# Kernel tuning notes

Hardware: AMD Instinct MI355X
Metric: run time of the kernel (lower is better)

Reference implementation:

```python
import jax, jax.numpy as jnp
import numpy as np

BANK_FILTERS = 64
DIM = 128
KSIZE = 3
BATCH = 256


def setup_inputs() -> dict:
    key = jax.random.key(0)
    k1, k2 = jax.random.split(key)
    bank_request = jax.random.normal(k1, (BATCH, BANK_FILTERS), dtype=jnp.float32)
    weight = jax.random.normal(k2, (BANK_FILTERS, DIM, DIM, KSIZE, KSIZE), dtype=jnp.float32)
    return {"bank_request": bank_request, "weight": weight}


def reference(bank_request, weight):
    # softmax over filter bank, then weighted sum of filters -> per-sample kernel
    probs = jax.nn.softmax(bank_request, axis=1)          # (B, F)
    Fb, D1, D2, K1, K2 = weight.shape
    # express as a single GEMM over the filter axis instead of broadcast-mul-reduce
    w2d = weight.reshape(Fb, D1 * D2 * K1 * K2)           # (F, D*D*k*k)
    kernel = probs @ w2d                                   # (B, D*D*k*k)
    return kernel.reshape(bank_request.shape[0], D1, D2, K1, K2)
```

## Files before the change

### kernel.cpp

```cpp
#include <hip/hip_runtime.h>
#include <math.h>

#define BATCH 256
#define FB    64
#define NCOL  147456
#define TPB   256
#define BT    32

#define FMA4(a, s, w) do { \
    (a).x = fmaf((s), (w).x, (a).x); \
    (a).y = fmaf((s), (w).y, (a).y); \
    (a).z = fmaf((s), (w).z, (a).z); \
    (a).w = fmaf((s), (w).w, (a).w); \
} while (0)

__global__ void softmax_rows(const float* __restrict__ x, float* __restrict__ p) {
    const int b = blockIdx.x;
    const int lane = threadIdx.x;
    float v = x[b * FB + lane];
    float m = v;
#pragma unroll
    for (int o = 32; o > 0; o >>= 1) m = fmaxf(m, __shfl_xor(m, o));
    float e = __expf(v - m);
    float s = e;
#pragma unroll
    for (int o = 32; o > 0; o >>= 1) s += __shfl_xor(s, o);
    p[b * FB + lane] = e / s;
}

__global__ __launch_bounds__(TPB, 2) void bank_gemm(
        const float* __restrict__ W, const float* __restrict__ P,
        float* __restrict__ out) {
    __shared__ float pt[FB * BT];

    const int tid = threadIdx.x;
    const int bg  = blockIdx.y;

    for (int i = tid; i < FB * BT; i += TPB) {
        const int f = i & (FB - 1);
        const int b = i >> 6;
        pt[f * BT + b] = P[bg * (FB * BT) + i];
    }
    __syncthreads();

    const int ncol4 = NCOL / 4;
    const float4* Wv = (const float4*)W;
    const int c4 = blockIdx.x * TPB + tid;

    float4 acc[BT];
#pragma unroll
    for (int b = 0; b < BT; ++b) acc[b] = make_float4(0.f, 0.f, 0.f, 0.f);

    float4 w = Wv[c4];
    for (int f = 0; f < FB; ++f) {
        float4 wn = w;
        if (f + 1 < FB) wn = Wv[(f + 1) * ncol4 + c4];
        const float4* p4 = (const float4*)&pt[f * BT];
#pragma unroll
        for (int q = 0; q < BT / 4; ++q) {
            const float4 p = p4[q];
            FMA4(acc[4 * q + 0], p.x, w);
            FMA4(acc[4 * q + 1], p.y, w);
            FMA4(acc[4 * q + 2], p.z, w);
            FMA4(acc[4 * q + 3], p.w, w);
        }
        w = wn;
    }

    float4* Ov = (float4*)out;
    const long long obase = (long long)(bg * BT) * ncol4 + c4;
#pragma unroll
    for (int b = 0; b < BT; ++b) {
        Ov[obase + (long long)b * ncol4] = acc[b];
    }
}

extern "C" void kernel_launch(void* const* d_in, const int* in_sizes, int n_in,
                              void* d_out, int out_size, void* d_ws, size_t ws_size,
                              hipStream_t stream) {
    const float* bank   = (const float*)d_in[0];
    const float* weight = (const float*)d_in[1];
    float* out   = (float*)d_out;
    float* probs = (float*)d_ws;

    softmax_rows<<<BATCH, FB, 0, stream>>>(bank, probs);

    dim3 grid(NCOL / (TPB * 4), BATCH / BT);
    bank_gemm<<<grid, TPB, 0, stream>>>(weight, probs, out);
}
```

Measured before the change: 217.6 us.

## Read transposed probs via scalar loads and use nontemporal output stores

The softmax kernel now writes probabilities transposed (filter-major), so the GEMM kernel can read them directly from global memory as wave-uniform scalar loads. This removes the shared-memory staging and the barrier. Output stores become nontemporal so the large write stream bypasses cache retention. Accumulation uses ext_vector_type float4. The GEMM is write-bound, with 151MB of output, so nontemporal stores may help. Scalar loads of probs add latency inside the f loop.

Measured after the change: 222.0 us. 1.02x slower.

```diff
diff --git a/kernel.cpp b/kernel.cpp
--- a/kernel.cpp
+++ b/kernel.cpp
@@ -7,14 +7,9 @@
 #define TPB   256
 #define BT    32
 
-#define FMA4(a, s, w) do { \
-    (a).x = fmaf((s), (w).x, (a).x); \
-    (a).y = fmaf((s), (w).y, (a).y); \
-    (a).z = fmaf((s), (w).z, (a).z); \
-    (a).w = fmaf((s), (w).w, (a).w); \
-} while (0)
+typedef float vfloat4 __attribute__((ext_vector_type(4)));
 
-__global__ void softmax_rows(const float* __restrict__ x, float* __restrict__ p) {
+__global__ void softmax_t(const float* __restrict__ x, float* __restrict__ pt) {
     const int b = blockIdx.x;
     const int lane = threadIdx.x;
     float v = x[b * FB + lane];
@@ -25,53 +20,41 @@
     float s = e;
 #pragma unroll
     for (int o = 32; o > 0; o >>= 1) s += __shfl_xor(s, o);
-    p[b * FB + lane] = e / s;
+    pt[lane * BATCH + b] = e / s;
 }
 
 __global__ __launch_bounds__(TPB, 2) void bank_gemm(
-        const float* __restrict__ W, const float* __restrict__ P,
+        const float* __restrict__ W, const float* __restrict__ PT,
         float* __restrict__ out) {
-    __shared__ float pt[FB * BT];
+    const int tid = threadIdx.x;
+    const int ncol4 = NCOL / 4;
+    const vfloat4* __restrict__ Wv = (const vfloat4*)W;
+    const int c4 = blockIdx.x * TPB + tid;
+    const int bg = blockIdx.y;
+    const float* __restrict__ P0 = PT + bg * BT;
 
-    const int tid = threadIdx.x;
-    const int bg  = blockIdx.y;
+    vfloat4 acc[BT];
+#pragma unroll
+    for (int b = 0; b < BT; ++b) acc[b] = (vfloat4)(0.f);
 
-    for (int i = tid; i < FB * BT; i += TPB) {
-        const int f = i & (FB - 1);
-        const int b = i >> 6;
-        pt[f * BT + b] = P[bg * (FB * BT) + i];
-    }
-    __syncthreads();
-
-    const int ncol4 = NCOL / 4;
-    const float4* Wv = (const float4*)W;
-    const int c4 = blockIdx.x * TPB + tid;
-
-    float4 acc[BT];
+    vfloat4 w = Wv[c4];
+    for (int f = 0; f < FB; ++f) {
+        vfloat4 wn = w;
+        if (f + 1 < FB) wn = Wv[(f + 1) * ncol4 + c4];
+        const float* __restrict__ pr = P0 + f * BATCH;
 #pragma unroll
-    for (int b = 0; b < BT; ++b) acc[b] = make_float4(0.f, 0.f, 0.f, 0.f);
-
-    float4 w = Wv[c4];
-    for (int f = 0; f < FB; ++f) {
-        float4 wn = w;
-        if (f + 1 < FB) wn = Wv[(f + 1) * ncol4 + c4];
-        const float4* p4 = (const float4*)&pt[f * BT];
-#pragma unroll
-        for (int q = 0; q < BT / 4; ++q) {
-            const float4 p = p4[q];
-            FMA4(acc[4 * q + 0], p.x, w);
-            FMA4(acc[4 * q + 1], p.y, w);
-            FMA4(acc[4 * q + 2], p.z, w);
-            FMA4(acc[4 * q + 3], p.w, w);
+        for (int b = 0; b < BT; ++b) {
+            const float p = pr[b];
+            acc[b] = w * p + acc[b];
         }
         w = wn;
     }
 
-    float4* Ov = (float4*)out;
+    vfloat4* Ov = (vfloat4*)out;
     const long long obase = (long long)(bg * BT) * ncol4 + c4;
 #pragma unroll
     for (int b = 0; b < BT; ++b) {
-        Ov[obase + (long long)b * ncol4] = acc[b];
+        __builtin_nontemporal_store(acc[b], &Ov[obase + (long long)b * ncol4]);
     }
 }
 
@@ -80,11 +63,11 @@
                               hipStream_t stream) {
     const float* bank   = (const float*)d_in[0];
     const float* weight = (const float*)d_in[1];
-    float* out   = (float*)d_out;
-    float* probs = (float*)d_ws;
+    float* out    = (float*)d_out;
+    float* probsT = (float*)d_ws;
 
-    softmax_rows<<<BATCH, FB, 0, stream>>>(bank, probs);
+    softmax_t<<<BATCH, FB, 0, stream>>>(bank, probsT);
 
     dim3 grid(NCOL / (TPB * 4), BATCH / BT);
-    bank_gemm<<<grid, TPB, 0, stream>>>(weight, probs, out);
+    bank_gemm<<<grid, TPB, 0, stream>>>(weight, probsT, out);
 }
```
